# Performance work log

Hardware: AMD Instinct MI355X
Metric: run time of the kernel (lower is better)

## Reference

```python
import jax, jax.numpy as jnp
import numpy as np

N, E, G, H, ED, L = 100000, 256000, 4000, 300, 64, 5
BN_EPS = 1e-5


def _bn(x, p):
    # p: [4, D] = (gamma, beta, running_mean, running_var); eval-mode batchnorm
    g, b, m, v = p[0], p[1], p[2], p[3]
    return (x - m) * (g / jnp.sqrt(v + BN_EPS)) + b


def setup_inputs() -> dict:
    key = jax.random.key(0)
    ks = iter(jax.random.split(key, 64))
    r = lambda *s: jax.random.normal(next(ks), s, jnp.float32) * 0.02

    def bn_pack(*s):
        # stacked (gamma, beta, mean, var) along axis -2
        return jnp.stack([jnp.ones(s, jnp.float32), jnp.zeros(s, jnp.float32),
                          jax.random.normal(next(ks), s, jnp.float32) * 0.1,
                          jnp.ones(s, jnp.float32)], axis=-2)

    inp = {
        'x': jax.random.randint(next(ks), (N,), 0, 119),
        'edge_attr': jax.random.randint(next(ks), (E,), 0, 32),
        'edge_index': jax.random.randint(next(ks), (2, E), 0, N),
        'batch': jnp.sort(jax.random.randint(next(ks), (N,), 0, G)),
        'num_graphs': G,
        # encoders
        'atom_emb': r(119, H), 'bond_emb': r(32, ED),
        # per-layer GINEConv params (stacked over L layers)
        'We': r(L, H, ED), 'be': jnp.zeros((L, H)),              # edge Linear(edge_dim->hidden)
        'W1': r(L, 2 * H, H), 'b1': jnp.zeros((L, 2 * H)), 'bn1': bn_pack(L, 2 * H),
        'W2': r(L, H, 2 * H), 'b2': jnp.zeros((L, H)), 'bn2': bn_pack(L, H),
        'eps': jnp.zeros((L,), jnp.float32),                      # trainable GIN eps, init 0
        # per-layer pooling linear
        'Wp': r(L, H, H), 'bp': jnp.zeros((L, H)),
        # virtual-node update MLP
        'vnW1': r(H, H), 'vnb1': jnp.zeros((H,)), 'vnbn': bn_pack(H),
        'vnW2': r(H, H), 'vnb2': jnp.zeros((H,)),
        # readout layernorm + head (Linear(H,H//2) -> SiLU -> Linear(H//2,1))
        'ln_g': jnp.ones((H,)), 'ln_b': jnp.zeros((H,)),
        'hW1': r(H // 2, H), 'hb1': jnp.zeros((H // 2,)),
        'hW2': r(1, H // 2), 'hb2': jnp.zeros((1,)),
    }
    return inp


def reference(x, edge_attr, edge_index, batch, num_graphs, atom_emb, bond_emb,
              We, be, W1, b1, bn1, W2, b2, bn2, eps, Wp, bp,
              vnW1, vnb1, vnbn, vnW2, vnb2, ln_g, ln_b, hW1, hb1, hW2, hb2):
    Gn = num_graphs
    h = atom_emb[x]                         # [N, H] atom encoding
    e = bond_emb[edge_attr]                 # [E, ED] bond encoding
    src, dst = edge_index[0], edge_index[1]
    Nn, Hd = h.shape
    vn = jnp.zeros((Gn, Hd), h.dtype)       # vn_embedding init to 0
    hg = jnp.zeros((Gn, Hd), h.dtype)       # sum-over-layers graph readout
    nlayers = We.shape[0]
    for i in range(nlayers):
        if i > 0:
            # virtual-node update + broadcast
            vn_in = jax.ops.segment_sum(h, batch, num_segments=Gn) + vn
            vn = jax.nn.silu(_bn(vn_in @ vnW1.T + vnb1, vnbn)) @ vnW2.T + vnb2
            h = h + vn[batch]
        # GINEConv: sum_j ReLU(h_j + lin(e_ij)) scattered into target nodes
        ep = e @ We[i].T + be[i]             # [E, H]
        m = jax.nn.relu(h[src] + ep)         # gather + relu
        agg = jax.ops.segment_sum(m, dst, num_segments=Nn)  # scatter-add
        z = (1.0 + eps[i]) * h + agg
        z = jax.nn.silu(_bn(z @ W1[i].T + b1[i], bn1[i])) @ W2[i].T + b2[i]  # 2-layer MLP
        z = jax.nn.silu(_bn(z, bn2[i]))      # layer BN + SiLU
        h = z + h if i > 0 else z            # residual (skipped at layer 0)
        hp = jax.ops.segment_sum(h, batch, num_segments=Gn)  # global_add_pool
        hg = hg + hp @ Wp[i].T + bp[i]
    # readout: LayerNorm -> SiLU -> head MLP
    mu = hg.mean(-1, keepdims=True)
    var = ((hg - mu) ** 2).mean(-1, keepdims=True)
    r = jax.nn.silu((hg - mu) / jnp.sqrt(var + BN_EPS) * ln_g + ln_b)
    return jax.nn.silu(r @ hW1.T + hb1) @ hW2.T + hb2   # [G, 1]
```

## Files before the change

### kernel.cpp

```cpp
#include <hip/hip_runtime.h>
#include <hip/hip_bf16.h>
#include <math.h>


typedef __hip_bfloat16 bf16;
typedef __attribute__((ext_vector_type(8))) __bf16 bf16x8;
typedef __attribute__((ext_vector_type(4))) float f32x4;

__device__ __forceinline__ float silu_f(float v) { return v / (1.0f + __expf(-v)); }

#define GLOAD16(gp, lp) __builtin_amdgcn_global_load_lds( \
    (const __attribute__((address_space(1))) unsigned int*)(const void*)(gp), \
    (__attribute__((address_space(3))) unsigned int*)(void*)(lp), 16, 0, 0)

__global__ void k_fill(float* __restrict__ p, float v, int n) {
    int stride = gridDim.x * blockDim.x;
    for (int i = blockIdx.x * blockDim.x + threadIdx.x; i < n; i += stride) p[i] = v;
}

__global__ void k_zero(float* __restrict__ p, size_t n) {
    size_t stride = (size_t)gridDim.x * blockDim.x;
    for (size_t i = (size_t)blockIdx.x * blockDim.x + threadIdx.x; i < n; i += stride)
        p[i] = 0.0f;
}

__global__ void k_hist(const int* __restrict__ key, int* __restrict__ cnt, int n) {
    int stride = gridDim.x * blockDim.x;
    for (int i = blockIdx.x * blockDim.x + threadIdx.x; i < n; i += stride)
        atomicAdd(&cnt[key[i]], 1);
}

__global__ __launch_bounds__(256)
void k_scan1(const int* __restrict__ in, int* __restrict__ out,
             int* __restrict__ bsum, int n) {
    __shared__ int wsum[4];
    int base = blockIdx.x << 10;
    int t = threadIdx.x;
    int i0 = base + t * 4;
    int v0 = (i0 + 0 < n) ? in[i0 + 0] : 0;
    int v1 = (i0 + 1 < n) ? in[i0 + 1] : 0;
    int v2 = (i0 + 2 < n) ? in[i0 + 2] : 0;
    int v3 = (i0 + 3 < n) ? in[i0 + 3] : 0;
    int s = v0 + v1 + v2 + v3;
    int lane = t & 63, wid = t >> 6;
    int x = s;
    for (int d = 1; d < 64; d <<= 1) {
        int y = __shfl_up(x, d);
        if (lane >= d) x += y;
    }
    if (lane == 63) wsum[wid] = x;
    __syncthreads();
    int wadd = 0;
    for (int w = 0; w < wid; w++) wadd += wsum[w];
    x += wadd;
    int run = x - s;
    if (i0 + 0 < n) out[i0 + 0] = run; run += v0;
    if (i0 + 1 < n) out[i0 + 1] = run; run += v1;
    if (i0 + 2 < n) out[i0 + 2] = run; run += v2;
    if (i0 + 3 < n) out[i0 + 3] = run; run += v3;
    if (bsum && t == 255) bsum[blockIdx.x] = x;
}

__global__ void k_scan_add(int* __restrict__ out, const int* __restrict__ bsum,
                           int* __restrict__ cur, int n, int total) {
    int stride = gridDim.x * blockDim.x;
    for (int i = blockIdx.x * blockDim.x + threadIdx.x; i < n; i += stride) {
        int v = out[i] + bsum[i >> 10];
        out[i] = v;
        if (cur) cur[i] = v;
    }
    if (blockIdx.x == 0 && threadIdx.x == 0) out[n] = total;
}

__global__ void k_escatter(const int* __restrict__ dst, const int* __restrict__ src,
                           const int* __restrict__ ea, int* __restrict__ cur,
                           int* __restrict__ esrc, int* __restrict__ eea, int E) {
    int stride = gridDim.x * blockDim.x;
    for (int e = blockIdx.x * blockDim.x + threadIdx.x; e < E; e += stride) {
        int p = atomicAdd(&cur[dst[e]], 1);
        esrc[p] = src[e];
        eea[p]  = ea[e];
    }
}

__global__ void k_eptable(const float* __restrict__ bond_emb,
                          const float* __restrict__ We,
                          const float* __restrict__ be,
                          float* __restrict__ tbl, int BV, int H, int ED) {
    int l = blockIdx.x / BV;
    int a = blockIdx.x % BV;
    int j = threadIdx.x;
    if (j >= H) return;
    const float* w = We + ((size_t)l * H + j) * ED;
    const float* bb = bond_emb + (size_t)a * ED;
    float s = be[(size_t)l * H + j];
    for (int k = 0; k < ED; k++) s += bb[k] * w[k];
    tbl[((size_t)l * BV + a) * H + j] = s;
}

__global__ void k_encode(const int* __restrict__ x, const float* __restrict__ emb,
                         bf16* __restrict__ h, int H, int total) {
    int stride = gridDim.x * blockDim.x;
    for (int i = blockIdx.x * blockDim.x + threadIdx.x; i < total; i += stride) {
        int n = i / H, j = i - n * H;
        h[i] = __float2bfloat16(emb[(size_t)x[n] * H + j]);
    }
}

__global__ __launch_bounds__(256)
void k_msg_csr(const int* __restrict__ eoff, const int* __restrict__ esrc,
               const int* __restrict__ eea, const bf16* __restrict__ h,
               const float* __restrict__ tbl, const float* __restrict__ epsp, int l,
               bf16* __restrict__ zb, int H, int KP1, int N) {
    const int wid = blockIdx.x * (blockDim.x >> 6) + (threadIdx.x >> 6);
    const int nw = gridDim.x * (blockDim.x >> 6);
    const int lane = threadIdx.x & 63;
    const float epl = 1.0f + epsp[l];
    for (int n = wid; n < N; n += nw) {
        int e0 = eoff[n], e1 = eoff[n + 1];
        float acc[5] = {0.f, 0.f, 0.f, 0.f, 0.f};
        for (int e = e0; e < e1; e++) {
            int s = esrc[e], a = eea[e];
            const bf16* hr = h + (size_t)s * H;
            const float* tr = tbl + (size_t)a * H;
            #pragma unroll
            for (int k = 0; k < 5; k++) {
                int j = lane + k * 64;
                if (j < H) {
                    float v = __bfloat162float(hr[j]) + tr[j];
                    if (v > 0.0f) acc[k] += v;
                }
            }
        }
        const bf16* hn = h + (size_t)n * H;
        #pragma unroll
        for (int k = 0; k < 5; k++) {
            int j = lane + k * 64;
            if (j >= KP1) continue;
            float z = 0.0f;
            if (j < H) z = epl * __bfloat162float(hn[j]) + acc[k];
            zb[(size_t)n * KP1 + j] = __float2bfloat16(z);
        }
    }
}

__global__ __launch_bounds__(320)
void k_pool_csr(const int* __restrict__ goff, const bf16* __restrict__ h,
                float* __restrict__ hp, bf16* __restrict__ hps, int layer, int KPS,
                int H, int G) {
    int j = threadIdx.x;
    if (j >= H) return;
    for (int g = blockIdx.x; g < G; g += gridDim.x) {
        float s = 0.0f;
        int n0 = goff[g], n1 = goff[g + 1];
        for (int n = n0; n < n1; n++)
            s += __bfloat162float(h[(size_t)n * H + j]);
        hp[(size_t)g * H + j] = s;
        hps[(size_t)g * KPS + layer * H + j] = __float2bfloat16(s);
    }
}

__global__ void k_addvn(bf16* __restrict__ h, const float* __restrict__ vn,
                        const int* __restrict__ batch, int H, int total) {
    int stride = gridDim.x * blockDim.x;
    for (int i = blockIdx.x * blockDim.x + threadIdx.x; i < total; i += stride) {
        int n = i / H, j = i - n * H;
        h[i] = __float2bfloat16(__bfloat162float(h[i]) + vn[(size_t)batch[n] * H + j]);
    }
}

__global__ void k_add_castpad(const float* __restrict__ hp, const float* __restrict__ vn,
                              bf16* __restrict__ o, int H, int KP, int total) {
    int stride = gridDim.x * blockDim.x;
    for (int i = blockIdx.x * blockDim.x + threadIdx.x; i < total; i += stride) {
        int g = i / KP, c = i - g * KP;
        float v = 0.0f;
        if (c < H) v = hp[(size_t)g * H + c] + vn[(size_t)g * H + c];
        o[i] = __float2bfloat16(v);
    }
}

__global__ void k_castw_all(const float* __restrict__ W, bf16* __restrict__ Wb,
                            int L, int R, int K, int Kp, int total) {
    int stride = gridDim.x * blockDim.x;
    int perL = R * K;
    for (int i = blockIdx.x * blockDim.x + threadIdx.x; i < total; i += stride) {
        int RpKp = total / L;
        int l = i / RpKp, rem = i - l * RpKp;
        int r = rem / Kp, c = rem - r * Kp;
        float v = (r < R && c < K) ? W[(size_t)l * perL + (size_t)r * K + c] : 0.0f;
        Wb[i] = __float2bfloat16(v);
    }
}

__global__ void k_castWps(const float* __restrict__ Wp, bf16* __restrict__ Wb,
                          int L, int H, int KPS, int total) {
    int stride = gridDim.x * blockDim.x;
    for (int i = blockIdx.x * blockDim.x + threadIdx.x; i < total; i += stride) {
        int r = i / KPS, c = i - r * KPS;
        float v = 0.0f;
        if (r < H && c < L * H) {
            int li = c / H, k = c - li * H;
            v = Wp[(size_t)li * H * H + (size_t)r * H + k];
        }
        Wb[i] = __float2bfloat16(v);
    }
}

__global__ void k_sumbias(const float* __restrict__ bp, float* __restrict__ o,
                          int L, int H) {
    int j = blockIdx.x * blockDim.x + threadIdx.x;
    if (j < H) {
        float s = 0.f;
        for (int i = 0; i < L; i++) s += bp[(size_t)i * H + j];
        o[j] = s;
    }
}

__global__ __launch_bounds__(512)
void k_mfma_gemm(const bf16* __restrict__ A, const bf16* __restrict__ B,
                 const float* __restrict__ bias, const float* __restrict__ bn,
                 const bf16* __restrict__ resb, bf16* __restrict__ out,
                 float* __restrict__ outf,
                 int M, int Nc, int Kp, int ldA, int ldOut, int ldPad,
                 int dosilu, int ncol) {
    __shared__ short As[2 * 128 * 32];
    __shared__ short Bs[2 * 128 * 32];
    const int nwg = gridDim.x;
    const int bid = blockIdx.x;
    const int q = nwg >> 3, r = nwg & 7;
    const int xcd = bid & 7, ii = bid >> 3;
    const int wgid = (xcd < r ? xcd * (q + 1) : r * (q + 1) + (xcd - r) * q) + ii;
    const int rb = wgid / ncol, cb = wgid - rb * ncol;
    const int bm = rb * 128, bn0 = cb * 128;

    const int tid = threadIdx.x;
    const int wave = tid >> 6, lane = tid & 63;
    const int wr = wave >> 1, wc = wave & 1;
    const int l15 = lane & 15, l4 = lane >> 4;
    const int srow = wave * 16 + (lane >> 2);
    const int sslot = lane & 3;

    f32x4 acc[2][4];
    #pragma unroll
    for (int mi = 0; mi < 2; mi++)
        #pragma unroll
        for (int ni = 0; ni < 4; ni++)
            acc[mi][ni] = (f32x4){0.f, 0.f, 0.f, 0.f};

    const int sg = (sslot ^ ((srow >> 1) & 3)) << 3;

    auto STAGE = [&](int buf, int k0) {
        GLOAD16(A + (size_t)(bm + srow) * ldA + k0 + sg, As + buf * 4096 + wave * 512);
        GLOAD16(B + (size_t)(bn0 + srow) * Kp + k0 + sg, Bs + buf * 4096 + wave * 512);
    };

    const int nt = Kp >> 5;
    STAGE(0, 0);
    for (int t = 0; t < nt; ++t) {
        if (t + 1 < nt) {
            STAGE((t + 1) & 1, (t + 1) << 5);
            asm volatile("s_waitcnt vmcnt(2)" ::: "memory");
        } else {
            asm volatile("s_waitcnt vmcnt(0)" ::: "memory");
        }
        __builtin_amdgcn_sched_barrier(0);
        __builtin_amdgcn_s_barrier();
        const short* Ab = As + (t & 1) * 4096;
        const short* Bb = Bs + (t & 1) * 4096;
        bf16x8 a[2], b[4];
        #pragma unroll
        for (int mi = 0; mi < 2; mi++) {
            int row = wr * 32 + mi * 16 + l15;
            a[mi] = *(const bf16x8*)&Ab[row * 32 + ((l4 ^ ((row >> 1) & 3)) << 3)];
        }
        #pragma unroll
        for (int ni = 0; ni < 4; ni++) {
            int row = wc * 64 + ni * 16 + l15;
            b[ni] = *(const bf16x8*)&Bb[row * 32 + ((l4 ^ ((row >> 1) & 3)) << 3)];
        }
        #pragma unroll
        for (int mi = 0; mi < 2; mi++)
            #pragma unroll
            for (int ni = 0; ni < 4; ni++)
                acc[mi][ni] = __builtin_amdgcn_mfma_f32_16x16x32_bf16(
                    a[mi], b[ni], acc[mi][ni], 0, 0, 0);
        __builtin_amdgcn_sched_barrier(0);
        __builtin_amdgcn_s_barrier();
    }

    #pragma unroll
    for (int ni = 0; ni < 4; ni++) {
        int col = bn0 + wc * 64 + ni * 16 + l15;
        if (col >= ldPad) continue;
        bool pad = (col >= Nc);
        float bi = (!pad && bias) ? bias[col] : 0.f;
        float sc = 1.f, mm = 0.f, bb = 0.f;
        if (!pad && bn) {
            sc = bn[col] * rsqrtf(bn[3 * Nc + col] + 1e-5f);
            mm = bn[2 * Nc + col];
            bb = bn[Nc + col];
        }
        #pragma unroll
        for (int mi = 0; mi < 2; mi++) {
            #pragma unroll
            for (int rr = 0; rr < 4; rr++) {
                int row = bm + wr * 32 + mi * 16 + l4 * 4 + rr;
                if (row >= M) continue;
                size_t idx = (size_t)row * ldOut + col;
                if (outf) {
                    if (pad) continue;
                    float v = acc[mi][ni][rr] + bi;
                    if (bn) v = (v - mm) * sc + bb;
                    if (dosilu) v = silu_f(v);
                    outf[idx] = v;
                } else {
                    if (pad) { out[idx] = __float2bfloat16(0.f); continue; }
                    float v = acc[mi][ni][rr] + bi;
                    if (bn) v = (v - mm) * sc + bb;
                    if (dosilu) v = silu_f(v);
                    if (resb) v += __bfloat162float(resb[idx]);
                    out[idx] = __float2bfloat16(v);
                }
            }
        }
    }
}

#define GBM 64
#define GBN 64
#define GBK 16
__global__ __launch_bounds__(256)
void k_gemm(const float* __restrict__ A, const float* __restrict__ B,
            const float* __restrict__ bias, const float* __restrict__ bn,
            float* __restrict__ C, int M, int Nc, int K, int flags) {
    __shared__ float As[GBK][GBM + 4];
    __shared__ float Bs[GBK][GBN + 4];
    const int bm = blockIdx.x * GBM;
    const int bnc = blockIdx.y * GBN;
    const int tid = threadIdx.x;
    const int tx = tid & 15, ty = tid >> 4;
    const int ar = tid >> 2;
    const int ak = (tid & 3) << 2;

    float acc[4][4] = {{0.f}};

    for (int k0 = 0; k0 < K; k0 += GBK) {
        {
            int gr = bm + ar, gk = k0 + ak;
            float4 v = make_float4(0.f, 0.f, 0.f, 0.f);
            if (gr < M && gk < K) {
                const float* p = A + (size_t)gr * K;
                if (gk + 3 < K) v = *(const float4*)(p + gk);
                else {
                    v.x = p[gk];
                    if (gk + 1 < K) v.y = p[gk + 1];
                    if (gk + 2 < K) v.z = p[gk + 2];
                }
            }
            As[ak][ar] = v.x; As[ak + 1][ar] = v.y; As[ak + 2][ar] = v.z; As[ak + 3][ar] = v.w;
        }
        {
            int gr = bnc + ar, gk = k0 + ak;
            float4 v = make_float4(0.f, 0.f, 0.f, 0.f);
            if (gr < Nc && gk < K) {
                const float* p = B + (size_t)gr * K;
                if (gk + 3 < K) v = *(const float4*)(p + gk);
                else {
                    v.x = p[gk];
                    if (gk + 1 < K) v.y = p[gk + 1];
                    if (gk + 2 < K) v.z = p[gk + 2];
                }
            }
            Bs[ak][ar] = v.x; Bs[ak + 1][ar] = v.y; Bs[ak + 2][ar] = v.z; Bs[ak + 3][ar] = v.w;
        }
        __syncthreads();
        #pragma unroll
        for (int kk = 0; kk < GBK; kk++) {
            float4 a = *(const float4*)&As[kk][ty * 4];
            float4 b = *(const float4*)&Bs[kk][tx * 4];
            acc[0][0] += a.x * b.x; acc[0][1] += a.x * b.y; acc[0][2] += a.x * b.z; acc[0][3] += a.x * b.w;
            acc[1][0] += a.y * b.x; acc[1][1] += a.y * b.y; acc[1][2] += a.y * b.z; acc[1][3] += a.y * b.w;
            acc[2][0] += a.z * b.x; acc[2][1] += a.z * b.y; acc[2][2] += a.z * b.z; acc[2][3] += a.z * b.w;
            acc[3][0] += a.w * b.x; acc[3][1] += a.w * b.y; acc[3][2] += a.w * b.z; acc[3][3] += a.w * b.w;
        }
        __syncthreads();
    }

    #pragma unroll
    for (int i = 0; i < 4; i++) {
        int row = bm + ty * 4 + i;
        if (row >= M) continue;
        #pragma unroll
        for (int j = 0; j < 4; j++) {
            int col = bnc + tx * 4 + j;
            if (col >= Nc) continue;
            float v = acc[i][j];
            if (bias) v += bias[col];
            if (bn) {
                float g = bn[col], bb = bn[Nc + col], mm = bn[2 * Nc + col], vv = bn[3 * Nc + col];
                v = (v - mm) * (g * rsqrtf(vv + 1e-5f)) + bb;
            }
            if (flags & 1) v = silu_f(v);
            size_t idx = (size_t)row * Nc + col;
            if (flags & 2) C[idx] += v;
            else           C[idx] = v;
        }
    }
}

__global__ __launch_bounds__(256)
void k_ln_silu(const float* __restrict__ hg, const float* __restrict__ g,
               const float* __restrict__ b, float* __restrict__ r, int H) {
    int gi = blockIdx.x;
    const float* row = hg + (size_t)gi * H;
    float s = 0.f, s2 = 0.f;
    for (int j = threadIdx.x; j < H; j += blockDim.x) {
        float v = row[j];
        s += v; s2 += v * v;
    }
    for (int off = 32; off; off >>= 1) {
        s += __shfl_down(s, off);
        s2 += __shfl_down(s2, off);
    }
    __shared__ float rs[4], rs2[4];
    int wid = threadIdx.x >> 6, lane = threadIdx.x & 63;
    if (lane == 0) { rs[wid] = s; rs2[wid] = s2; }
    __syncthreads();
    if (threadIdx.x == 0) {
        float S = 0.f, S2 = 0.f;
        for (int w = 0; w < 4; w++) { S += rs[w]; S2 += rs2[w]; }
        rs[0] = S; rs2[0] = S2;
    }
    __syncthreads();
    float mu = rs[0] / H;
    float var = rs2[0] / H - mu * mu;
    float inv = rsqrtf(var + 1e-5f);
    for (int j = threadIdx.x; j < H; j += blockDim.x) {
        float v = (row[j] - mu) * inv * g[j] + b[j];
        r[(size_t)gi * H + j] = silu_f(v);
    }
}

__global__ void k_head2(const float* __restrict__ r2, const float* __restrict__ w,
                        const float* __restrict__ b, float* __restrict__ out, int Kh) {
    int gi = blockIdx.x;
    int t = threadIdx.x;
    float s = 0.f;
    for (int k = t; k < Kh; k += 64) s += r2[(size_t)gi * Kh + k] * w[k];
    for (int off = 32; off; off >>= 1) s += __shfl_down(s, off);
    if (t == 0) out[gi] = s + b[0];
}

extern "C" void kernel_launch(void* const* d_in, const int* in_sizes, int n_in,
                              void* d_out, int out_size, void* d_ws, size_t ws_size,
                              hipStream_t stream) {
    const int*   x         = (const int*)d_in[0];
    const int*   edge_attr = (const int*)d_in[1];
    const int*   eidx      = (const int*)d_in[2];
    const int*   batch     = (const int*)d_in[3];
    const float* atom_emb  = (const float*)d_in[5];
    const float* bond_emb  = (const float*)d_in[6];
    const float* We  = (const float*)d_in[7];
    const float* be  = (const float*)d_in[8];
    const float* W1  = (const float*)d_in[9];
    const float* b1  = (const float*)d_in[10];
    const float* bn1 = (const float*)d_in[11];
    const float* W2  = (const float*)d_in[12];
    const float* b2  = (const float*)d_in[13];
    const float* bn2 = (const float*)d_in[14];
    const float* epsp= (const float*)d_in[15];
    const float* Wp  = (const float*)d_in[16];
    const float* bp  = (const float*)d_in[17];
    const float* vnW1= (const float*)d_in[18];
    const float* vnb1= (const float*)d_in[19];
    const float* vnbn= (const float*)d_in[20];
    const float* vnW2= (const float*)d_in[21];
    const float* vnb2= (const float*)d_in[22];
    const float* ln_g= (const float*)d_in[23];
    const float* ln_b= (const float*)d_in[24];
    const float* hW1 = (const float*)d_in[25];
    const float* hb1 = (const float*)d_in[26];
    const float* hW2 = (const float*)d_in[27];
    const float* hb2 = (const float*)d_in[28];
    float* out = (float*)d_out;

    const int N  = in_sizes[0];
    const int E  = in_sizes[1];
    const int G  = out_size;
    const int L  = in_sizes[15];
    const int H  = in_sizes[19];
    const int H2 = 2 * H;
    const int ED = in_sizes[7] / (L * H);
    const int BV = in_sizes[6] / ED;
    const int HH = in_sizes[26];
    (void)n_in;

    const int* src = eidx;
    const int* dst = eidx + E;

    const int KP1 = ((H  + 31) / 32) * 32;
    const int KP2 = ((H2 + 31) / 32) * 32;
    const int KPS = ((L * H + 31) / 32) * 32;
    const int RP1 = ((H2 + 127) / 128) * 128;
    const int RP2 = ((H  + 127) / 128) * 128;
    const int Npad = ((N + 127) / 128) * 128;
    const int GP   = ((G + 127) / 128) * 128;

    char* wsb = (char*)d_ws;
    auto alb = [](size_t v) { return (v + 255) & ~(size_t)255; };
    const size_t fN = (size_t)N * H;
    const size_t fG = (size_t)G * H;

    size_t off = 0;
    bf16*  hbf   = (bf16*) (wsb + off); off += alb(fN * 2);
    bf16*  zb    = (bf16*) (wsb + off); off += alb((size_t)Npad * KP1 * 2);
    float* hp    = (float*)(wsb + off); off += alb(fG * 4);
    float* hg    = (float*)(wsb + off); off += alb(fG * 4);
    float* vn    = (float*)(wsb + off); off += alb(fG * 4);
    float* rbuf  = (float*)(wsb + off); off += alb(fG * 4);
    float* r2    = (float*)(wsb + off); off += alb((size_t)G * HH * 4);
    float* tbl   = (float*)(wsb + off); off += alb((size_t)L * BV * H * 4);
    float* bsumf = (float*)(wsb + off); off += alb((size_t)RP2 * 4);
    bf16*  W1b   = (bf16*) (wsb + off); off += alb((size_t)L * RP1 * KP1 * 2);
    bf16*  W2b   = (bf16*) (wsb + off); off += alb((size_t)L * RP2 * KP2 * 2);
    bf16*  vnW1b = (bf16*) (wsb + off); off += alb((size_t)RP2 * KP1 * 2);
    bf16*  vnW2b = (bf16*) (wsb + off); off += alb((size_t)RP2 * KP1 * 2);
    bf16*  Wpsb  = (bf16*) (wsb + off); off += alb((size_t)RP2 * KPS * 2);
    bf16*  hps   = (bf16*) (wsb + off); off += alb((size_t)GP * KPS * 2);
    bf16*  vninb = (bf16*) (wsb + off); off += alb((size_t)GP * KP1 * 2);
    bf16*  vntb  = (bf16*) (wsb + off); off += alb((size_t)GP * KP1 * 2);
    int* eoff = (int*)(wsb + off); off += alb((size_t)(N + 1) * 4);
    int* ecur = (int*)(wsb + off); off += alb((size_t)N * 4);
    int* esrc = (int*)(wsb + off); off += alb((size_t)E * 4);
    int* eea  = (int*)(wsb + off); off += alb((size_t)E * 4);
    int* goff = (int*)(wsb + off); off += alb((size_t)(G + 1) * 4);
    int* gcnt = (int*)(wsb + off); off += alb((size_t)G * 4);
    int* bsum = (int*)(wsb + off); off += alb(1024 * 4);

    size_t left = (ws_size > off + 256) ? (ws_size - off - 256) : 0;
    long long chl = (long long)(left / ((size_t)KP2 * 2));
    int CH = (int)((chl > Npad) ? Npad : chl);
    CH = (CH / 128) * 128;
    if (CH < 128) {
        k_fill<<<64, 256, 0, stream>>>(out, 10000.0f + (float)(ws_size >> 20), G);
        return;
    }
    bf16* t1 = (bf16*)(wsb + off);

    auto gemm_f = [&](const float* A, const float* B, const float* bias, const float* bn,
                      float* C, int M, int Nc, int K, int flags) {
        dim3 grid((M + GBM - 1) / GBM, (Nc + GBN - 1) / GBN);
        k_gemm<<<grid, dim3(256), 0, stream>>>(A, B, bias, bn, C, M, Nc, K, flags);
    };
    auto mfma = [&](const bf16* A, const bf16* B, const float* bias, const float* bn,
                    const bf16* resb, bf16* outb, float* outf, int M, int Nc, int Kp,
                    int ldA, int ldOut, int ldPad, int dosilu, int ncolT) {
        int mt = (M + 127) / 128;
        k_mfma_gemm<<<dim3(mt * ncolT), dim3(512), 0, stream>>>(
            A, B, bias, bn, resb, outb, outf, M, Nc, Kp, ldA, ldOut, ldPad, dosilu, ncolT);
    };
    auto zero = [&](void* p, size_t nfloats) { k_zero<<<1024, 256, 0, stream>>>((float*)p, nfloats); };

    const int NH = N * H;

    {
        int nb = (N + 1023) / 1024;
        zero(ecur, N);
        k_hist<<<1024, 256, 0, stream>>>(dst, ecur, E);
        k_scan1<<<nb, 256, 0, stream>>>(ecur, eoff, bsum, N);
        k_scan1<<<1, 256, 0, stream>>>(bsum, bsum, nullptr, nb);
        k_scan_add<<<512, 256, 0, stream>>>(eoff, bsum, ecur, N, E);
        k_escatter<<<1024, 256, 0, stream>>>(dst, src, edge_attr, ecur, esrc, eea, E);

        int nbg = (G + 1023) / 1024;
        zero(gcnt, G);
        k_hist<<<1024, 256, 0, stream>>>(batch, gcnt, N);
        k_scan1<<<nbg, 256, 0, stream>>>(gcnt, goff, bsum, G);
        k_scan1<<<1, 256, 0, stream>>>(bsum, bsum, nullptr, nbg);
        k_scan_add<<<64, 256, 0, stream>>>(goff, bsum, nullptr, G, N);
    }

    zero(vn, fG);
    zero(hps, (size_t)GP * KPS / 2);

    k_eptable<<<L * BV, 320, 0, stream>>>(bond_emb, We, be, tbl, BV, H, ED);
    k_encode<<<2048, 256, 0, stream>>>(x, atom_emb, hbf, H, NH);
    k_castw_all<<<2048, 256, 0, stream>>>(W1, W1b, L, H2, H, KP1, L * RP1 * KP1);
    k_castw_all<<<2048, 256, 0, stream>>>(W2, W2b, L, H, H2, KP2, L * RP2 * KP2);
    k_castw_all<<<256, 256, 0, stream>>>(vnW1, vnW1b, 1, H, H, KP1, RP2 * KP1);
    k_castw_all<<<256, 256, 0, stream>>>(vnW2, vnW2b, 1, H, H, KP1, RP2 * KP1);
    k_castWps<<<512, 256, 0, stream>>>(Wp, Wpsb, L, H, KPS, RP2 * KPS);
    k_sumbias<<<(H + 255) / 256, 256, 0, stream>>>(bp, bsumf, L, H);

    for (int i = 0; i < L; i++) {
        if (i > 0) {
            k_add_castpad<<<2048, 256, 0, stream>>>(hp, vn, vninb, H, KP1, G * KP1);
            mfma(vninb, vnW1b, vnb1, vnbn, nullptr, vntb, nullptr,
                 G, H, KP1, KP1, KP1, KP1, 1, RP2 / 128);
            mfma(vntb, vnW2b, vnb2, nullptr, nullptr, nullptr, vn,
                 G, H, KP1, KP1, H, H, 0, RP2 / 128);
            k_addvn<<<2048, 256, 0, stream>>>(hbf, vn, batch, H, NH);
        }
        k_msg_csr<<<2048, 256, 0, stream>>>(eoff, esrc, eea, hbf,
                                            tbl + (size_t)i * BV * H, epsp, i,
                                            zb, H, KP1, N);
        for (int r0 = 0; r0 < N; r0 += CH) {
            int m = (N - r0 < CH) ? (N - r0) : CH;
            mfma(zb + (size_t)r0 * KP1, W1b + (size_t)i * RP1 * KP1,
                 b1 + (size_t)i * H2, bn1 + (size_t)i * 4 * H2,
                 nullptr, t1, nullptr, m, H2, KP1, KP1, KP2, KP2, 1, RP1 / 128);
            mfma(t1, W2b + (size_t)i * RP2 * KP2, b2 + (size_t)i * H,
                 bn2 + (size_t)i * 4 * H,
                 (i > 0) ? (hbf + (size_t)r0 * H) : nullptr, hbf + (size_t)r0 * H,
                 nullptr, m, H, KP2, KP2, H, H, 1, RP2 / 128);
        }
        k_pool_csr<<<4096, KP1, 0, stream>>>(goff, hbf, hp, hps, i, KPS, H, G);
    }

    mfma(hps, Wpsb, bsumf, nullptr, nullptr, nullptr, hg,
         G, H, KPS, KPS, H, H, 0, RP2 / 128);

    k_ln_silu<<<G, 256, 0, stream>>>(hg, ln_g, ln_b, rbuf, H);
    gemm_f(rbuf, hW1, hb1, nullptr, r2, G, HH, H, 1);
    k_head2<<<G, 64, 0, stream>>>(r2, hW2, hb2, out, HH);
}
```

Before: 2.478 ms.

## Vectorize bf16 pairs in message/pool/addvn, bf16 edge table, triple-buffer GEMM

The message, pooling and virtual-node-add kernels now read and write two bf16 values per 32-bit access instead of single elements. The edge projection table is stored as padded bf16 rather than fp32, which halves gather traffic at a small precision cost. The MFMA GEMM moves from a double-buffered to a triple-buffered LDS pipeline, which drops one barrier per k-step but raises LDS use per block. The message kernel grid is also doubled.

Result: faster. 2.228 ms, median of 2 (-10.1%).

```diff
diff --git a/kernel.cpp b/kernel.cpp
--- a/kernel.cpp
+++ b/kernel.cpp
@@ -8,6 +8,16 @@
 typedef __attribute__((ext_vector_type(4))) float f32x4;
 
 __device__ __forceinline__ float silu_f(float v) { return v / (1.0f + __expf(-v)); }
+__device__ __forceinline__ float bfu_lo(unsigned u) {
+    unsigned t = (u & 0xffffu) << 16; return *(float*)&t;
+}
+__device__ __forceinline__ float bfu_hi(unsigned u) {
+    unsigned t = u & 0xffff0000u; return *(float*)&t;
+}
+__device__ __forceinline__ unsigned packbf(float a, float b) {
+    bf16 x = __float2bfloat16(a), y = __float2bfloat16(b);
+    return (unsigned)*(unsigned short*)&x | ((unsigned)*(unsigned short*)&y << 16);
+}
 
 #define GLOAD16(gp, lp) __builtin_amdgcn_global_load_lds( \
     (const __attribute__((address_space(1))) unsigned int*)(const void*)(gp), \
@@ -86,16 +96,19 @@
 __global__ void k_eptable(const float* __restrict__ bond_emb,
                           const float* __restrict__ We,
                           const float* __restrict__ be,
-                          float* __restrict__ tbl, int BV, int H, int ED) {
+                          bf16* __restrict__ tblb, int BV, int H, int ED, int KP1) {
     int l = blockIdx.x / BV;
     int a = blockIdx.x % BV;
     int j = threadIdx.x;
-    if (j >= H) return;
-    const float* w = We + ((size_t)l * H + j) * ED;
-    const float* bb = bond_emb + (size_t)a * ED;
-    float s = be[(size_t)l * H + j];
-    for (int k = 0; k < ED; k++) s += bb[k] * w[k];
-    tbl[((size_t)l * BV + a) * H + j] = s;
+    if (j >= KP1) return;
+    float s = 0.0f;
+    if (j < H) {
+        const float* w = We + ((size_t)l * H + j) * ED;
+        const float* bb = bond_emb + (size_t)a * ED;
+        s = be[(size_t)l * H + j];
+        for (int k = 0; k < ED; k++) s += bb[k] * w[k];
+    }
+    tblb[((size_t)l * BV + a) * KP1 + j] = __float2bfloat16(s);
 }
 
 __global__ void k_encode(const int* __restrict__ x, const float* __restrict__ emb,
@@ -110,62 +123,84 @@
 __global__ __launch_bounds__(256)
 void k_msg_csr(const int* __restrict__ eoff, const int* __restrict__ esrc,
                const int* __restrict__ eea, const bf16* __restrict__ h,
-               const float* __restrict__ tbl, const float* __restrict__ epsp, int l,
+               const bf16* __restrict__ tblb, const float* __restrict__ epsp, int l,
                bf16* __restrict__ zb, int H, int KP1, int N) {
     const int wid = blockIdx.x * (blockDim.x >> 6) + (threadIdx.x >> 6);
     const int nw = gridDim.x * (blockDim.x >> 6);
     const int lane = threadIdx.x & 63;
     const float epl = 1.0f + epsp[l];
+    const int c0 = 2 * lane;
     for (int n = wid; n < N; n += nw) {
         int e0 = eoff[n], e1 = eoff[n + 1];
-        float acc[5] = {0.f, 0.f, 0.f, 0.f, 0.f};
+        float a0[3] = {0.f, 0.f, 0.f}, a1[3] = {0.f, 0.f, 0.f};
         for (int e = e0; e < e1; e++) {
             int s = esrc[e], a = eea[e];
-            const bf16* hr = h + (size_t)s * H;
-            const float* tr = tbl + (size_t)a * H;
+            const unsigned short* hr = (const unsigned short*)h + (size_t)s * H;
+            const unsigned short* tr = (const unsigned short*)tblb + (size_t)a * KP1;
             #pragma unroll
-            for (int k = 0; k < 5; k++) {
-                int j = lane + k * 64;
-                if (j < H) {
-                    float v = __bfloat162float(hr[j]) + tr[j];
-                    if (v > 0.0f) acc[k] += v;
+            for (int p = 0; p < 3; p++) {
+                int c = c0 + p * 128;
+                if (c < H) {
+                    unsigned hv = *(const unsigned*)(hr + c);
+                    unsigned tv = *(const unsigned*)(tr + c);
+                    float v0 = bfu_lo(hv) + bfu_lo(tv);
+                    float v1 = bfu_hi(hv) + bfu_hi(tv);
+                    if (v0 > 0.0f) a0[p] += v0;
+                    if (v1 > 0.0f) a1[p] += v1;
                 }
             }
         }
-        const bf16* hn = h + (size_t)n * H;
-        #pragma unroll
-        for (int k = 0; k < 5; k++) {
-            int j = lane + k * 64;
-            if (j >= KP1) continue;
-            float z = 0.0f;
-            if (j < H) z = epl * __bfloat162float(hn[j]) + acc[k];
-            zb[(size_t)n * KP1 + j] = __float2bfloat16(z);
-        }
-    }
-}
-
-__global__ __launch_bounds__(320)
+        const unsigned short* hn = (const unsigned short*)h + (size_t)n * H;
+        unsigned short* zr = (unsigned short*)zb + (size_t)n * KP1;
+        #pragma unroll
+        for (int p = 0; p < 3; p++) {
+            int c = c0 + p * 128;
+            if (c < KP1) {
+                float z0 = 0.f, z1 = 0.f;
+                if (c < H) {
+                    unsigned hv = *(const unsigned*)(hn + c);
+                    z0 = epl * bfu_lo(hv) + a0[p];
+                    z1 = epl * bfu_hi(hv) + a1[p];
+                }
+                *(unsigned*)(zr + c) = packbf(z0, z1);
+            }
+        }
+    }
+}
+
+__global__ __launch_bounds__(256)
 void k_pool_csr(const int* __restrict__ goff, const bf16* __restrict__ h,
                 float* __restrict__ hp, bf16* __restrict__ hps, int layer, int KPS,
                 int H, int G) {
     int j = threadIdx.x;
-    if (j >= H) return;
+    int c = 2 * j;
+    if (c >= H) return;
     for (int g = blockIdx.x; g < G; g += gridDim.x) {
-        float s = 0.0f;
+        float s0 = 0.0f, s1 = 0.0f;
         int n0 = goff[g], n1 = goff[g + 1];
-        for (int n = n0; n < n1; n++)
-            s += __bfloat162float(h[(size_t)n * H + j]);
-        hp[(size_t)g * H + j] = s;
-        hps[(size_t)g * KPS + layer * H + j] = __float2bfloat16(s);
+        const unsigned short* hb = (const unsigned short*)h;
+        for (int n = n0; n < n1; n++) {
+            unsigned hv = *(const unsigned*)(hb + (size_t)n * H + c);
+            s0 += bfu_lo(hv);
+            s1 += bfu_hi(hv);
+        }
+        hp[(size_t)g * H + c] = s0;
+        hp[(size_t)g * H + c + 1] = s1;
+        *(unsigned*)((unsigned short*)hps + (size_t)g * KPS + layer * H + c) = packbf(s0, s1);
     }
 }
 
 __global__ void k_addvn(bf16* __restrict__ h, const float* __restrict__ vn,
-                        const int* __restrict__ batch, int H, int total) {
-    int stride = gridDim.x * blockDim.x;
-    for (int i = blockIdx.x * blockDim.x + threadIdx.x; i < total; i += stride) {
-        int n = i / H, j = i - n * H;
-        h[i] = __float2bfloat16(__bfloat162float(h[i]) + vn[(size_t)batch[n] * H + j]);
+                        const int* __restrict__ batch, int H, int total2) {
+    int stride = gridDim.x * blockDim.x;
+    int HP = H >> 1;
+    for (int i = blockIdx.x * blockDim.x + threadIdx.x; i < total2; i += stride) {
+        int n = i / HP, p = i - n * HP;
+        int c = 2 * p;
+        unsigned short* hr = (unsigned short*)h + (size_t)n * H + c;
+        unsigned hv = *(unsigned*)hr;
+        const float* vr = vn + (size_t)batch[n] * H + c;
+        *(unsigned*)hr = packbf(bfu_lo(hv) + vr[0], bfu_hi(hv) + vr[1]);
     }
 }
 
@@ -224,8 +259,8 @@
                  float* __restrict__ outf,
                  int M, int Nc, int Kp, int ldA, int ldOut, int ldPad,
                  int dosilu, int ncol) {
-    __shared__ short As[2 * 128 * 32];
-    __shared__ short Bs[2 * 128 * 32];
+    __shared__ short As[3 * 128 * 32];
+    __shared__ short Bs[3 * 128 * 32];
     const int nwg = gridDim.x;
     const int bid = blockIdx.x;
     const int q = nwg >> 3, r = nwg & 7;
@@ -257,17 +292,16 @@
 
     const int nt = Kp >> 5;
     STAGE(0, 0);
+    if (nt > 1) STAGE(1, 32);
     for (int t = 0; t < nt; ++t) {
-        if (t + 1 < nt) {
-            STAGE((t + 1) & 1, (t + 1) << 5);
-            asm volatile("s_waitcnt vmcnt(2)" ::: "memory");
-        } else {
-            asm volatile("s_waitcnt vmcnt(0)" ::: "memory");
-        }
+        if (t + 1 < nt) asm volatile("s_waitcnt vmcnt(2)" ::: "memory");
+        else            asm volatile("s_waitcnt vmcnt(0)" ::: "memory");
         __builtin_amdgcn_sched_barrier(0);
         __builtin_amdgcn_s_barrier();
-        const short* Ab = As + (t & 1) * 4096;
-        const short* Bb = Bs + (t & 1) * 4096;
+        __builtin_amdgcn_sched_barrier(0);
+        if (t + 2 < nt) STAGE((t + 2) % 3, (t + 2) << 5);
+        const short* Ab = As + (t % 3) * 4096;
+        const short* Bb = Bs + (t % 3) * 4096;
         bf16x8 a[2], b[4];
         #pragma unroll
         for (int mi = 0; mi < 2; mi++) {
@@ -286,7 +320,6 @@
                 acc[mi][ni] = __builtin_amdgcn_mfma_f32_16x16x32_bf16(
                     a[mi], b[ni], acc[mi][ni], 0, 0, 0);
         __builtin_amdgcn_sched_barrier(0);
-        __builtin_amdgcn_s_barrier();
     }
 
     #pragma unroll
@@ -520,7 +553,7 @@
     float* vn    = (float*)(wsb + off); off += alb(fG * 4);
     float* rbuf  = (float*)(wsb + off); off += alb(fG * 4);
     float* r2    = (float*)(wsb + off); off += alb((size_t)G * HH * 4);
-    float* tbl   = (float*)(wsb + off); off += alb((size_t)L * BV * H * 4);
+    bf16*  tblb  = (bf16*) (wsb + off); off += alb((size_t)L * BV * KP1 * 2);
     float* bsumf = (float*)(wsb + off); off += alb((size_t)RP2 * 4);
     bf16*  W1b   = (bf16*) (wsb + off); off += alb((size_t)L * RP1 * KP1 * 2);
     bf16*  W2b   = (bf16*) (wsb + off); off += alb((size_t)L * RP2 * KP2 * 2);
@@ -584,7 +617,7 @@
     zero(vn, fG);
     zero(hps, (size_t)GP * KPS / 2);
 
-    k_eptable<<<L * BV, 320, 0, stream>>>(bond_emb, We, be, tbl, BV, H, ED);
+    k_eptable<<<L * BV, 320, 0, stream>>>(bond_emb, We, be, tblb, BV, H, ED, KP1);
     k_encode<<<2048, 256, 0, stream>>>(x, atom_emb, hbf, H, NH);
     k_castw_all<<<2048, 256, 0, stream>>>(W1, W1b, L, H2, H, KP1, L * RP1 * KP1);
     k_castw_all<<<2048, 256, 0, stream>>>(W2, W2b, L, H, H2, KP2, L * RP2 * KP2);
@@ -600,10 +633,10 @@
                  G, H, KP1, KP1, KP1, KP1, 1, RP2 / 128);
             mfma(vntb, vnW2b, vnb2, nullptr, nullptr, nullptr, vn,
                  G, H, KP1, KP1, H, H, 0, RP2 / 128);
-            k_addvn<<<2048, 256, 0, stream>>>(hbf, vn, batch, H, NH);
-        }
-        k_msg_csr<<<2048, 256, 0, stream>>>(eoff, esrc, eea, hbf,
-                                            tbl + (size_t)i * BV * H, epsp, i,
+            k_addvn<<<2048, 256, 0, stream>>>(hbf, vn, batch, H, N * (H >> 1));
+        }
+        k_msg_csr<<<4096, 256, 0, stream>>>(eoff, esrc, eea, hbf,
+                                            tblb + (size_t)i * BV * KP1, epsp, i,
                                             zb, H, KP1, N);
         for (int r0 = 0; r0 < N; r0 += CH) {
             int m = (N - r0 < CH) ? (N - r0) : CH;
@@ -615,7 +648,7 @@
                  (i > 0) ? (hbf + (size_t)r0 * H) : nullptr, hbf + (size_t)r0 * H,
                  nullptr, m, H, KP2, KP2, H, H, 1, RP2 / 128);
         }
-        k_pool_csr<<<4096, KP1, 0, stream>>>(goff, hbf, hp, hps, i, KPS, H, G);
+        k_pool_csr<<<4096, 256, 0, stream>>>(goff, hbf, hp, hps, i, KPS, H, G);
     }
 
     mfma(hps, Wpsb, bsumf, nullptr, nullptr, nullptr, hg,
```
